# Kernel optimization log

Hardware: AMD Instinct MI355X
Metric: run time of the kernel (lower is better)

Reference implementation:

```python
import jax, jax.numpy as jnp
import numpy as np

B, N, F_IN, OUT_FEATS, NUM_CLS, NUM_INDS = 256, 200, 200, 256, 8, 512
PCT_EDGES = 20
K = int(PCT_EDGES / 100 * N * (N - 1) / 2)  # 3980 hard edges
TAU = 1.0


def setup_inputs() -> dict:
    key = jax.random.key(0)
    ks = jax.random.split(key, 6)
    x = jax.random.normal(ks[0], (B, N, F_IN), dtype=jnp.float32)
    gumbel_u = jax.random.uniform(ks[1], (B, N, N), dtype=jnp.float32)
    nets = jax.random.normal(ks[2], (NUM_INDS, N, N), dtype=jnp.float32)
    w_gnn = jax.random.normal(ks[3], (F_IN, OUT_FEATS), dtype=jnp.float32) / np.sqrt(F_IN).astype(np.float32)
    w_lin = jax.random.normal(ks[4], (OUT_FEATS, NUM_CLS), dtype=jnp.float32) / np.sqrt(OUT_FEATS).astype(np.float32)
    b_lin = jnp.zeros((NUM_CLS,), dtype=jnp.float32)
    net_index = jax.random.randint(ks[5], (B,), 0, NUM_INDS)
    return {"x": x, "gumbel_u": gumbel_u, "nets": nets, "w_gnn": w_gnn,
            "w_lin": w_lin, "b_lin": b_lin, "net_index": net_index}


def _gumbel_softkmax(logits, u, k, tau):
    # logits: [B, N, N]; u: uniform(0,1) noise -> Gumbel(0,1) via -log(-log(u))
    b, n, _ = logits.shape
    g = -jnp.log(-jnp.log(jnp.clip(u, 1e-10, 1.0 - 1e-10)))
    g = (logits + g) / tau
    sym = (g + jnp.swapaxes(g, 1, 2)) * 0.5                      # symmetrize
    y_soft = jax.nn.softmax(sym.reshape(b, -1), axis=-1).reshape(b, n, n)
    upper_flat = jnp.triu(y_soft).reshape(b, -1)                 # upper tri incl. diag
    _, idx = jax.lax.top_k(upper_flat, k)                        # [B, k]
    y_hard = jnp.zeros_like(upper_flat).at[jnp.arange(b)[:, None], idx].set(1.0)
    y_hard = y_hard.reshape(b, n, n)
    diag = jnp.diagonal(y_hard, axis1=-2, axis2=-1)              # [B, N]
    eye = jnp.eye(n, dtype=y_hard.dtype)
    y_hard = y_hard + jnp.swapaxes(y_hard, 1, 2) - diag[:, :, None] * eye
    # straight-through estimator
    return y_hard - jax.lax.stop_gradient(y_soft) + y_soft


def reference(x, gumbel_u, nets, w_gnn, w_lin, b_lin, net_index):
    selected = nets[net_index]                                   # [B, N, N]
    adj = _gumbel_softkmax(selected, gumbel_u, K, TAU)
    # gnn: relu(adj @ x @ W_gnn)  -> embeddings [B, N, OUT_FEATS]
    emb = jax.nn.relu(jnp.einsum('bij,bjf,fo->bio', adj, x, w_gnn))
    out = emb @ w_lin + b_lin                                    # [B, N, NUM_CLS]
    return out, emb, adj
```

## Files before the change

kernel.cpp:

```cpp
#include <hip/hip_runtime.h>
#include <math.h>

#define B_SZ 256
#define N_SZ 200
#define NN (N_SZ * N_SZ)
#define FIN 200
#define OUT_F 256
#define NCLS 8
#define KSEL 3980
#define NUPPER 20100
#define KSTRIDE 20128
#define NT 7
#define NTILES 28
#define CAND_CAP 2048

#define ADJ_STRIDE 224
#define KGRP_PB 25
#define XWM_PB (KGRP_PB * 2048)

#define EMB_OFF (B_SZ * N_SZ * NCLS)
#define ADJ_OFF (EMB_OFF + B_SZ * N_SZ * OUT_F)

#define KEYS_OFF_B   0
#define SEL_OFF_B    21659648
#define CCNT_OFF_B   21661696
#define CAND_OFF_B   21662720
#define WKG_OFF_B    26214400
#define ADJB16_OFF_B 26329088

typedef unsigned short ushort_t;
typedef float f32x4 __attribute__((ext_vector_type(4)));
typedef short bf16x8 __attribute__((ext_vector_type(8)));
typedef ushort_t u16x4 __attribute__((ext_vector_type(4)));

__device__ __forceinline__ unsigned sortkey(float f) {
    unsigned u = __float_as_uint(f);
    return (u & 0x80000000u) ? ~u : (u | 0x80000000u);
}

__device__ __forceinline__ ushort_t f2b(float f) {
    unsigned u = __float_as_uint(f);
    return (ushort_t)((u + 0x7FFFu + ((u >> 16) & 1u)) >> 16);
}

__device__ __forceinline__ bf16x8 f2b8(float4 lo, float4 hi) {
    bf16x8 r;
    r[0] = (short)f2b(lo.x); r[1] = (short)f2b(lo.y);
    r[2] = (short)f2b(lo.z); r[3] = (short)f2b(lo.w);
    r[4] = (short)f2b(hi.x); r[5] = (short)f2b(hi.y);
    r[6] = (short)f2b(hi.z); r[7] = (short)f2b(hi.w);
    return r;
}

__device__ __forceinline__ void tile_decode(int t, int& ti, int& tj) {
    int a = 0, rem = t;
    while (rem >= NT - a) { rem -= NT - a; ++a; }
    ti = a; tj = a + rem;
}

__global__ __launch_bounds__(256) void kA(
    const float* __restrict__ gu, const float* __restrict__ nets,
    const int* __restrict__ net_index, unsigned* __restrict__ keys,
    const float* __restrict__ wg, ushort_t* __restrict__ wkg,
    unsigned* __restrict__ candCnt)
{
    const int blk = blockIdx.x;
    if (blk >= B_SZ * NTILES) {
        int pb = blk - B_SZ * NTILES;
        if (pb == 0) candCnt[threadIdx.x] = 0;
        int e = pb * 256 + threadIdx.x;
        int kg = e >> 11;
        int rem = e & 2047;
        int n = rem >> 3;
        int ki = rem & 7;
        int k = kg * 8 + ki;
        wkg[e] = (k < FIN) ? f2b(wg[k * OUT_F + n]) : (ushort_t)0;
        return;
    }
    const int b = blk / NTILES;
    int ti, tj; tile_decode(blk % NTILES, ti, tj);
    const int i0 = ti * 32, j0 = tj * 32;
    const float* ub = gu + (size_t)b * NN;
    const float* lb = nets + (size_t)net_index[b] * NN;

    __shared__ float Hij[32][33];
    __shared__ float Hji[32][33];

    const int r = threadIdx.x >> 5;
    const int c = threadIdx.x & 31;

    #pragma unroll
    for (int s = 0; s < 4; ++s) {
        int rr = r + 8 * s;
        int i = i0 + rr, j = j0 + c;
        if (i < N_SZ && j < N_SZ) {
            float u = ub[i * N_SZ + j];
            u = fminf(fmaxf(u, 1e-10f), 1.0f - 1e-10f);
            Hij[rr][c] = lb[i * N_SZ + j] - logf(-logf(u));
        }
        if (ti != tj) {
            int i2 = j0 + rr, j2 = i0 + c;
            if (i2 < N_SZ && j2 < N_SZ) {
                float u = ub[i2 * N_SZ + j2];
                u = fminf(fmaxf(u, 1e-10f), 1.0f - 1e-10f);
                Hji[rr][c] = lb[i2 * N_SZ + j2] - logf(-logf(u));
            }
        }
    }
    __syncthreads();

    unsigned* kb = keys + (size_t)b * KSTRIDE;
    #pragma unroll
    for (int s = 0; s < 4; ++s) {
        int rr = r + 8 * s;
        int i = i0 + rr, j = j0 + c;
        if (i < N_SZ && j < N_SZ && i <= j) {
            float hji = (ti == tj) ? Hij[c][rr] : Hji[c][rr];
            float sv = 0.5f * (Hij[rr][c] + hji);
            int base = i * N_SZ - (i * (i - 1)) / 2;
            kb[base + (j - i)] = sortkey(sv);
        }
    }
}

__global__ __launch_bounds__(256) void kFinal(
    const unsigned* __restrict__ keys, unsigned* __restrict__ sel)
{
    const int b = blockIdx.x;
    const int tid = threadIdx.x;
    __shared__ unsigned kl[NUPPER];
    __shared__ unsigned hist[256];
    __shared__ unsigned sfx[256];
    __shared__ unsigned sPrefix;
    __shared__ int sKK;

    const unsigned* kb = keys + (size_t)b * KSTRIDE;
    for (int idx = tid; idx < NUPPER; idx += 256) kl[idx] = kb[idx];

    unsigned prefix = 0;
    int kk = KSEL;
    for (int round = 0; round < 4; ++round) {
        const int shift = 24 - 8 * round;
        hist[tid] = 0;
        __syncthreads();
        for (int idx = tid; idx < NUPPER; idx += 256) {
            unsigned key = kl[idx];
            bool in = (round == 0) || ((key >> (shift + 8)) == prefix);
            if (in) atomicAdd(&hist[(key >> shift) & 255u], 1u);
        }
        __syncthreads();
        sfx[tid] = hist[tid];
        __syncthreads();
        #pragma unroll
        for (int off = 1; off < 256; off <<= 1) {
            unsigned add = (tid + off < 256) ? sfx[tid + off] : 0u;
            __syncthreads();
            sfx[tid] += add;
            __syncthreads();
        }
        unsigned above = (tid < 255) ? sfx[tid + 1] : 0u;
        if (sfx[tid] >= (unsigned)kk && above < (unsigned)kk) {
            sPrefix = (prefix << 8) | (unsigned)tid;
            sKK = kk - (int)above;
        }
        __syncthreads();
        prefix = sPrefix;
        kk = sKK;
        __syncthreads();
    }
    if (tid == 0) {
        sel[b * 2] = prefix;
        sel[b * 2 + 1] = (unsigned)kk;
    }
}

__global__ __launch_bounds__(256) void kW(
    const unsigned* __restrict__ keys, const unsigned* __restrict__ sel,
    unsigned* __restrict__ candCnt, unsigned* __restrict__ cand,
    float* __restrict__ out_base, ushort_t* __restrict__ adjb16)
{
    const int blk = blockIdx.x;
    const int b = blk / NTILES;
    int ti, tj; tile_decode(blk % NTILES, ti, tj);
    const int i0 = ti * 32, j0 = tj * 32;
    const unsigned kth = sel[b * 2];
    const unsigned* kb = keys + (size_t)b * KSTRIDE;
    float* adj = out_base + ADJ_OFF + (size_t)b * NN;
    ushort_t* ab = adjb16 + (size_t)b * (N_SZ * ADJ_STRIDE);

    __shared__ float V[32][33];
    const int r = threadIdx.x >> 5;
    const int c = threadIdx.x & 31;

    #pragma unroll
    for (int s = 0; s < 4; ++s) {
        int rr = r + 8 * s;
        int i = i0 + rr, j = j0 + c;
        if (i < N_SZ && j < N_SZ && i <= j) {
            int base = i * N_SZ - (i * (i - 1)) / 2;
            unsigned key = kb[base + (j - i)];
            float v = (key > kth) ? 1.0f : 0.0f;
            if (key == kth) {
                unsigned p = atomicAdd(&candCnt[b], 1u);
                if (p < CAND_CAP) cand[(size_t)b * CAND_CAP + p] = (unsigned)(i * N_SZ + j);
            }
            V[rr][c] = v;
            if (ti == tj) V[c][rr] = v;
        }
    }
    __syncthreads();

    const int tr = threadIdx.x >> 3;
    const int tc = threadIdx.x & 7;
    {
        int i = i0 + tr;
        if (i < N_SZ) {
            int jb = j0 + tc * 4;
            float v0 = (jb + 0 < N_SZ) ? V[tr][tc * 4 + 0] : 0.0f;
            float v1 = (jb + 1 < N_SZ) ? V[tr][tc * 4 + 1] : 0.0f;
            float v2 = (jb + 2 < N_SZ) ? V[tr][tc * 4 + 2] : 0.0f;
            float v3 = (jb + 3 < N_SZ) ? V[tr][tc * 4 + 3] : 0.0f;
            if (jb + 3 < N_SZ) {
                float4 v4 = {v0, v1, v2, v3};
                *(float4*)(adj + (size_t)i * N_SZ + jb) = v4;
            } else {
                if (jb + 0 < N_SZ) adj[(size_t)i * N_SZ + jb + 0] = v0;
                if (jb + 1 < N_SZ) adj[(size_t)i * N_SZ + jb + 1] = v1;
                if (jb + 2 < N_SZ) adj[(size_t)i * N_SZ + jb + 2] = v2;
            }
            u16x4 a4;
            a4[0] = (v0 != 0.0f) ? (ushort_t)0x3F80 : (ushort_t)0;
            a4[1] = (v1 != 0.0f) ? (ushort_t)0x3F80 : (ushort_t)0;
            a4[2] = (v2 != 0.0f) ? (ushort_t)0x3F80 : (ushort_t)0;
            a4[3] = (v3 != 0.0f) ? (ushort_t)0x3F80 : (ushort_t)0;
            *(u16x4*)(ab + (size_t)i * ADJ_STRIDE + jb) = a4;
        }
    }
    if (ti != tj) {
        int i2 = j0 + tr;
        if (i2 < N_SZ) {
            int jb = i0 + tc * 4;
            float v0 = V[tc * 4 + 0][tr];
            float v1 = V[tc * 4 + 1][tr];
            float v2 = V[tc * 4 + 2][tr];
            float v3 = V[tc * 4 + 3][tr];
            float4 v4 = {v0, v1, v2, v3};
            *(float4*)(adj + (size_t)i2 * N_SZ + jb) = v4;
            u16x4 a4;
            a4[0] = (v0 != 0.0f) ? (ushort_t)0x3F80 : (ushort_t)0;
            a4[1] = (v1 != 0.0f) ? (ushort_t)0x3F80 : (ushort_t)0;
            a4[2] = (v2 != 0.0f) ? (ushort_t)0x3F80 : (ushort_t)0;
            a4[3] = (v3 != 0.0f) ? (ushort_t)0x3F80 : (ushort_t)0;
            *(u16x4*)(ab + (size_t)i2 * ADJ_STRIDE + jb) = a4;
        }
    }
}

__global__ void kT(const unsigned* __restrict__ sel,
                   const unsigned* __restrict__ candCnt,
                   const unsigned* __restrict__ cand,
                   float* __restrict__ out_base, ushort_t* __restrict__ adjb16)
{
    const int b = blockIdx.x;
    if (threadIdx.x != 0) return;
    int kk = (int)sel[b * 2 + 1];
    int cnt = (int)candCnt[b];
    if (cnt > CAND_CAP) cnt = CAND_CAP;
    float* adj = out_base + ADJ_OFF + (size_t)b * NN;
    ushort_t* ab = adjb16 + (size_t)b * (N_SZ * ADJ_STRIDE);
    int take = kk < cnt ? kk : cnt;
    unsigned used[64];
    int nu = 0;
    for (int t = 0; t < take; ++t) {
        unsigned best = 0xFFFFFFFFu;
        for (int q = 0; q < cnt; ++q) {
            unsigned v = cand[(size_t)b * CAND_CAP + q];
            bool skip = false;
            for (int u = 0; u < nu; ++u) if (used[u] == v) { skip = true; break; }
            if (!skip && v < best) best = v;
        }
        if (best == 0xFFFFFFFFu) break;
        if (nu < 64) used[nu++] = best;
        int i = (int)(best / N_SZ), j = (int)(best % N_SZ);
        adj[i * N_SZ + j] = 1.0f;
        adj[j * N_SZ + i] = 1.0f;
        ab[i * ADJ_STRIDE + j] = (ushort_t)0x3F80;
        ab[j * ADJ_STRIDE + i] = (ushort_t)0x3F80;
    }
}

__global__ __launch_bounds__(256) void k2_mfma(
    const float* __restrict__ x, const ushort_t* __restrict__ wkg,
    ushort_t* __restrict__ xwm)
{
    const int r0 = blockIdx.x * 64;
    const int tid = threadIdx.x;
    const int w = tid >> 6;
    const int l = tid & 63;
    const int g = l >> 4;
    const int r = l & 15;

    __shared__ __align__(16) ushort_t Cs[64 * 256];

    f32x4 acc[4][4];
    #pragma unroll
    for (int mf = 0; mf < 4; ++mf)
        #pragma unroll
        for (int nf = 0; nf < 4; ++nf)
            acc[mf][nf] = (f32x4){0.f, 0.f, 0.f, 0.f};

    for (int c = 0; c < 7; ++c) {
        const int koff = (c * 32 + g * 8 < FIN) ? (c * 32 + g * 8) : 0;
        bf16x8 af[4], bf[4];
        #pragma unroll
        for (int mf = 0; mf < 4; ++mf) {
            const float* ap = x + (size_t)(r0 + mf * 16 + r) * FIN + koff;
            float4 lo = *(const float4*)ap;
            float4 hi = *(const float4*)(ap + 4);
            af[mf] = f2b8(lo, hi);
        }
        #pragma unroll
        for (int nf = 0; nf < 4; ++nf)
            bf[nf] = *(const bf16x8*)(wkg + c * 8192 + g * 2048 + (w * 64 + nf * 16 + r) * 8);
        #pragma unroll
        for (int mf = 0; mf < 4; ++mf)
            #pragma unroll
            for (int nf = 0; nf < 4; ++nf)
                acc[mf][nf] = __builtin_amdgcn_mfma_f32_16x16x32_bf16(
                    af[mf], bf[nf], acc[mf][nf], 0, 0, 0);
    }

    #pragma unroll
    for (int mf = 0; mf < 4; ++mf) {
        #pragma unroll
        for (int jj = 0; jj < 4; ++jj) {
            int row = mf * 16 + g * 4 + jj;
            #pragma unroll
            for (int nf = 0; nf < 4; ++nf) {
                int col = w * 64 + nf * 16 + r;
                Cs[((row >> 3) << 11) + col * 8 + (row & 7)] = f2b(acc[mf][nf][jj]);
            }
        }
    }
    __syncthreads();
    #pragma unroll
    for (int kg = 0; kg < 8; ++kg) {
        int grow0 = r0 + kg * 8;
        int bb = grow0 / N_SZ;
        int jb = grow0 % N_SZ;
        ushort_t* dst = xwm + (size_t)bb * XWM_PB + ((jb >> 3) << 11);
        *(int4*)(dst + tid * 8) = *(const int4*)(Cs + (kg << 11) + tid * 8);
    }
}

__global__ __launch_bounds__(256) void k3_fused(
    const ushort_t* __restrict__ adjb16, const ushort_t* __restrict__ xwm,
    const float* __restrict__ wl, const float* __restrict__ bl,
    float* __restrict__ out_base)
{
    const int blk = blockIdx.x;
    const int xcd = blk & 7;
    const int idx = blk >> 3;
    const int b = xcd + 8 * (idx / 7);
    const int mt = idx % 7;
    const int tid = threadIdx.x;
    const int w = tid >> 6;
    const int l = tid & 63;
    const int g = l >> 4;
    const int r = l & 15;

    const ushort_t* adjb = adjb16 + (size_t)b * (N_SZ * ADJ_STRIDE);
    const ushort_t* xwb = xwm + (size_t)b * XWM_PB;

    __shared__ __align__(16) float Es[32 * 256];
    float (*red)[4][8][8] = (float(*)[4][8][8])Es;

    int arow0 = mt * 32 + r;       if (arow0 > N_SZ - 1) arow0 = N_SZ - 1;
    int arow1 = mt * 32 + 16 + r;  if (arow1 > N_SZ - 1) arow1 = N_SZ - 1;
    bf16x8 aa[2][7];
    #pragma unroll
    for (int c = 0; c < 7; ++c) {
        aa[0][c] = *(const bf16x8*)(adjb + arow0 * ADJ_STRIDE + c * 32 + g * 8);
        aa[1][c] = *(const bf16x8*)(adjb + arow1 * ADJ_STRIDE + c * 32 + g * 8);
    }

    f32x4 acc[2][4];
    #pragma unroll
    for (int mf = 0; mf < 2; ++mf)
        #pragma unroll
        for (int nf = 0; nf < 4; ++nf)
            acc[mf][nf] = (f32x4){0.f, 0.f, 0.f, 0.f};

    #pragma unroll
    for (int c = 0; c < 7; ++c) {
        bf16x8 bf[4];
        #pragma unroll
        for (int nf = 0; nf < 4; ++nf)
            bf[nf] = *(const bf16x8*)(xwb + c * 8192 + g * 2048 + (w * 64 + nf * 16 + r) * 8);
        #pragma unroll
        for (int mf = 0; mf < 2; ++mf)
            #pragma unroll
            for (int nf = 0; nf < 4; ++nf)
                acc[mf][nf] = __builtin_amdgcn_mfma_f32_16x16x32_bf16(
                    aa[mf][c], bf[nf], acc[mf][nf], 0, 0, 0);
    }

    #pragma unroll
    for (int mf = 0; mf < 2; ++mf) {
        #pragma unroll
        for (int j = 0; j < 4; ++j) {
            int rowl = mf * 16 + g * 4 + j;
            #pragma unroll
            for (int nf = 0; nf < 4; ++nf)
                Es[rowl * 256 + w * 64 + nf * 16 + r] = fmaxf(acc[mf][nf][j], 0.0f);
        }
    }
    __syncthreads();
    #pragma unroll
    for (int q = 0; q < 8; ++q) {
        int e = q * 256 + tid;
        int rowl = e >> 6;
        int c4 = e & 63;
        int grow = mt * 32 + rowl;
        if (grow < N_SZ) {
            float4 v = *(const float4*)(Es + rowl * 256 + c4 * 4);
            *(float4*)(out_base + EMB_OFF + ((size_t)b * N_SZ + grow) * OUT_F + c4 * 4) = v;
        }
    }
    __syncthreads();

    float wlv[4][NCLS];
    #pragma unroll
    for (int nf = 0; nf < 4; ++nf) {
        int col = w * 64 + nf * 16 + r;
        #pragma unroll
        for (int cls = 0; cls < NCLS; ++cls) wlv[nf][cls] = wl[col * NCLS + cls];
    }
    #pragma unroll
    for (int mf = 0; mf < 2; ++mf) {
        #pragma unroll
        for (int j = 0; j < 4; ++j) {
            float e0 = fmaxf(acc[mf][0][j], 0.0f);
            float e1 = fmaxf(acc[mf][1][j], 0.0f);
            float e2 = fmaxf(acc[mf][2][j], 0.0f);
            float e3 = fmaxf(acc[mf][3][j], 0.0f);
            float pr[NCLS];
            #pragma unroll
            for (int cls = 0; cls < NCLS; ++cls)
                pr[cls] = e0 * wlv[0][cls] + e1 * wlv[1][cls]
                        + e2 * wlv[2][cls] + e3 * wlv[3][cls];
            #pragma unroll
            for (int off = 1; off <= 8; off <<= 1) {
                #pragma unroll
                for (int cls = 0; cls < NCLS; ++cls)
                    pr[cls] += __shfl_xor(pr[cls], off, 64);
            }
            if (r < NCLS) red[w][g][mf * 4 + j][r] = pr[r];
        }
    }
    __syncthreads();

    {
        int rowl = tid >> 3, cls = tid & 7;
        int mf = rowl >> 4, rem = rowl & 15, gg = rem >> 2, jj = rem & 3;
        int slot = mf * 4 + jj;
        int grow = mt * 32 + rowl;
        if (grow < N_SZ) {
            float s = red[0][gg][slot][cls] + red[1][gg][slot][cls]
                    + red[2][gg][slot][cls] + red[3][gg][slot][cls] + bl[cls];
            out_base[((size_t)b * N_SZ + grow) * NCLS + cls] = s;
        }
    }
}

extern "C" void kernel_launch(void* const* d_in, const int* in_sizes, int n_in,
                              void* d_out, int out_size, void* d_ws, size_t ws_size,
                              hipStream_t stream) {
    const float* x    = (const float*)d_in[0];
    const float* gu   = (const float*)d_in[1];
    const float* nets = (const float*)d_in[2];
    const float* wg   = (const float*)d_in[3];
    const float* wl   = (const float*)d_in[4];
    const float* bl   = (const float*)d_in[5];
    const int*   nidx = (const int*)d_in[6];
    float* out = (float*)d_out;

    char* ws = (char*)d_ws;
    unsigned* keys    = (unsigned*)(ws + KEYS_OFF_B);
    unsigned* sel     = (unsigned*)(ws + SEL_OFF_B);
    unsigned* candCnt = (unsigned*)(ws + CCNT_OFF_B);
    unsigned* cand    = (unsigned*)(ws + CAND_OFF_B);
    ushort_t* xwm     = (ushort_t*)(ws + KEYS_OFF_B);
    ushort_t* wkg     = (ushort_t*)(ws + WKG_OFF_B);
    ushort_t* adjb16  = (ushort_t*)(ws + ADJB16_OFF_B);

    kA<<<B_SZ * NTILES + 224, 256, 0, stream>>>(gu, nets, nidx, keys, wg, wkg, candCnt);
    kFinal<<<B_SZ, 256, 0, stream>>>(keys, sel);
    kW<<<B_SZ * NTILES, 256, 0, stream>>>(keys, sel, candCnt, cand, out, adjb16);
    kT<<<B_SZ, 64, 0, stream>>>(sel, candCnt, cand, out, adjb16);

    k2_mfma<<<(B_SZ * N_SZ) / 64, 256, 0, stream>>>(x, wkg, xwm);
    k3_fused<<<B_SZ * 7, 256, 0, stream>>>(adjb16, xwm, wl, bl, out);
}
```

Measured before the change: 148.4 us.

## Fuse x@W and adj@(xW) GEMMs into one per-batch kernel via LDS

Merges the two GEMM kernels into a single kernel with one block per batch. The block computes x@W_gnn for all 200 rows into registers, stages the bf16 result in swizzled shared memory, then multiplies by the adjacency and writes the embeddings and logits directly. This drops the global round trip of the intermediate xW and one launch. In exchange the grid shrinks to 256 large blocks with heavy register use (two 13x4 accumulator sets) and ~118KB of LDS, which limits occupancy and latency hiding. Embedding stores are now scalar and no longer staged through LDS.

Measured after the change: 224.1 us. +51.0%, slower.

```diff
diff --git a/kernel.cpp b/kernel.cpp
--- a/kernel.cpp
+++ b/kernel.cpp
@@ -15,8 +15,6 @@
 #define CAND_CAP 2048
 
 #define ADJ_STRIDE 224
-#define KGRP_PB 25
-#define XWM_PB (KGRP_PB * 2048)
 
 #define EMB_OFF (B_SZ * N_SZ * NCLS)
 #define ADJ_OFF (EMB_OFF + B_SZ * N_SZ * OUT_F)
@@ -41,15 +39,6 @@
 __device__ __forceinline__ ushort_t f2b(float f) {
     unsigned u = __float_as_uint(f);
     return (ushort_t)((u + 0x7FFFu + ((u >> 16) & 1u)) >> 16);
-}
-
-__device__ __forceinline__ bf16x8 f2b8(float4 lo, float4 hi) {
-    bf16x8 r;
-    r[0] = (short)f2b(lo.x); r[1] = (short)f2b(lo.y);
-    r[2] = (short)f2b(lo.z); r[3] = (short)f2b(lo.w);
-    r[4] = (short)f2b(hi.x); r[5] = (short)f2b(hi.y);
-    r[6] = (short)f2b(hi.z); r[7] = (short)f2b(hi.w);
-    return r;
 }
 
 __device__ __forceinline__ void tile_decode(int t, int& ti, int& tj) {
@@ -289,145 +278,145 @@
     }
 }
 
-__global__ __launch_bounds__(256) void k2_mfma(
+__global__ __launch_bounds__(256, 1) void k23(
     const float* __restrict__ x, const ushort_t* __restrict__ wkg,
-    ushort_t* __restrict__ xwm)
+    const ushort_t* __restrict__ adjb16, const float* __restrict__ wl,
+    const float* __restrict__ bl, float* __restrict__ out_base)
 {
-    const int r0 = blockIdx.x * 64;
+    const int b = blockIdx.x;
     const int tid = threadIdx.x;
     const int w = tid >> 6;
     const int l = tid & 63;
     const int g = l >> 4;
     const int r = l & 15;
 
-    __shared__ __align__(16) ushort_t Cs[64 * 256];
-
-    f32x4 acc[4][4];
-    #pragma unroll
-    for (int mf = 0; mf < 4; ++mf)
+    __shared__ __align__(16) char pool[118400];
+    ushort_t* Axs = (ushort_t*)(pool + 102400);
+
+    const float* xb = x + (size_t)b * (N_SZ * FIN);
+    const ushort_t* adjb = adjb16 + (size_t)b * (N_SZ * ADJ_STRIDE);
+
+    f32x4 acc1[13][4];
+    #pragma unroll
+    for (int mf = 0; mf < 13; ++mf)
         #pragma unroll
         for (int nf = 0; nf < 4; ++nf)
-            acc[mf][nf] = (f32x4){0.f, 0.f, 0.f, 0.f};
+            acc1[mf][nf] = (f32x4){0.f, 0.f, 0.f, 0.f};
+
+    float4 xr[7];
+    #pragma unroll
+    for (int i = 0; i < 7; ++i) {
+        int q = i * 256 + tid;
+        if (q < 1600)
+            xr[i] = *(const float4*)(xb + (size_t)(q >> 3) * FIN + (q & 7) * 4);
+    }
 
     for (int c = 0; c < 7; ++c) {
-        const int koff = (c * 32 + g * 8 < FIN) ? (c * 32 + g * 8) : 0;
-        bf16x8 af[4], bf[4];
-        #pragma unroll
-        for (int mf = 0; mf < 4; ++mf) {
-            const float* ap = x + (size_t)(r0 + mf * 16 + r) * FIN + koff;
-            float4 lo = *(const float4*)ap;
-            float4 hi = *(const float4*)(ap + 4);
-            af[mf] = f2b8(lo, hi);
-        }
+        __syncthreads();
+        #pragma unroll
+        for (int i = 0; i < 7; ++i) {
+            int q = i * 256 + tid;
+            if (q < 1600) {
+                int row = q >> 3, c4 = q & 7;
+                u16x4 v4;
+                v4[0] = f2b(xr[i].x); v4[1] = f2b(xr[i].y);
+                v4[2] = f2b(xr[i].z); v4[3] = f2b(xr[i].w);
+                *(u16x4*)(Axs + row * 40 + c4 * 4) = v4;
+            }
+        }
+        __syncthreads();
+        if (c < 6) {
+            int cn = c + 1;
+            #pragma unroll
+            for (int i = 0; i < 7; ++i) {
+                int q = i * 256 + tid;
+                if (q < 1600) {
+                    int col = cn * 32 + (q & 7) * 4;
+                    if (col < FIN)
+                        xr[i] = *(const float4*)(xb + (size_t)(q >> 3) * FIN + col);
+                    else
+                        xr[i] = (float4){0.f, 0.f, 0.f, 0.f};
+                }
+            }
+        }
+        bf16x8 bf[4];
         #pragma unroll
         for (int nf = 0; nf < 4; ++nf)
             bf[nf] = *(const bf16x8*)(wkg + c * 8192 + g * 2048 + (w * 64 + nf * 16 + r) * 8);
         #pragma unroll
-        for (int mf = 0; mf < 4; ++mf)
+        for (int mf = 0; mf < 13; ++mf) {
+            int row = mf * 16 + r; if (row > N_SZ - 1) row = N_SZ - 1;
+            bf16x8 af = *(const bf16x8*)(Axs + row * 40 + g * 8);
             #pragma unroll
             for (int nf = 0; nf < 4; ++nf)
-                acc[mf][nf] = __builtin_amdgcn_mfma_f32_16x16x32_bf16(
-                    af[mf], bf[nf], acc[mf][nf], 0, 0, 0);
-    }
-
-    #pragma unroll
-    for (int mf = 0; mf < 4; ++mf) {
-        #pragma unroll
-        for (int jj = 0; jj < 4; ++jj) {
-            int row = mf * 16 + g * 4 + jj;
-            #pragma unroll
-            for (int nf = 0; nf < 4; ++nf) {
-                int col = w * 64 + nf * 16 + r;
-                Cs[((row >> 3) << 11) + col * 8 + (row & 7)] = f2b(acc[mf][nf][jj]);
-            }
-        }
-    }
-    __syncthreads();
-    #pragma unroll
-    for (int kg = 0; kg < 8; ++kg) {
-        int grow0 = r0 + kg * 8;
-        int bb = grow0 / N_SZ;
-        int jb = grow0 % N_SZ;
-        ushort_t* dst = xwm + (size_t)bb * XWM_PB + ((jb >> 3) << 11);
-        *(int4*)(dst + tid * 8) = *(const int4*)(Cs + (kg << 11) + tid * 8);
-    }
-}
-
-__global__ __launch_bounds__(256) void k3_fused(
-    const ushort_t* __restrict__ adjb16, const ushort_t* __restrict__ xwm,
-    const float* __restrict__ wl, const float* __restrict__ bl,
-    float* __restrict__ out_base)
-{
-    const int blk = blockIdx.x;
-    const int xcd = blk & 7;
-    const int idx = blk >> 3;
-    const int b = xcd + 8 * (idx / 7);
-    const int mt = idx % 7;
-    const int tid = threadIdx.x;
-    const int w = tid >> 6;
-    const int l = tid & 63;
-    const int g = l >> 4;
-    const int r = l & 15;
-
-    const ushort_t* adjb = adjb16 + (size_t)b * (N_SZ * ADJ_STRIDE);
-    const ushort_t* xwb = xwm + (size_t)b * XWM_PB;
-
-    __shared__ __align__(16) float Es[32 * 256];
-    float (*red)[4][8][8] = (float(*)[4][8][8])Es;
-
-    int arow0 = mt * 32 + r;       if (arow0 > N_SZ - 1) arow0 = N_SZ - 1;
-    int arow1 = mt * 32 + 16 + r;  if (arow1 > N_SZ - 1) arow1 = N_SZ - 1;
-    bf16x8 aa[2][7];
+                acc1[mf][nf] = __builtin_amdgcn_mfma_f32_16x16x32_bf16(
+                    af, bf[nf], acc1[mf][nf], 0, 0, 0);
+        }
+    }
+
+    __syncthreads();
+    #pragma unroll
+    for (int mf = 0; mf < 13; ++mf) {
+        #pragma unroll
+        for (int j = 0; j < 4; ++j) {
+            int row = mf * 16 + g * 4 + j;
+            if (row < N_SZ) {
+                int kg = row >> 3;
+                int ki = row & 7;
+                #pragma unroll
+                for (int nf = 0; nf < 4; ++nf) {
+                    int col = w * 64 + nf * 16 + r;
+                    int byte = kg * 4096 + ((col ^ (kg & 7)) << 4) + ki * 2;
+                    *(ushort_t*)(pool + byte) = f2b(acc1[mf][nf][j]);
+                }
+            }
+        }
+    }
+    __syncthreads();
+
+    f32x4 acc2[13][4];
+    #pragma unroll
+    for (int mf = 0; mf < 13; ++mf)
+        #pragma unroll
+        for (int nf = 0; nf < 4; ++nf)
+            acc2[mf][nf] = (f32x4){0.f, 0.f, 0.f, 0.f};
+
+    bf16x8 ar[2][13];
+    #pragma unroll
+    for (int mf = 0; mf < 13; ++mf) {
+        int row = mf * 16 + r; if (row > N_SZ - 1) row = N_SZ - 1;
+        ar[0][mf] = *(const bf16x8*)(adjb + row * ADJ_STRIDE + g * 8);
+    }
     #pragma unroll
     for (int c = 0; c < 7; ++c) {
-        aa[0][c] = *(const bf16x8*)(adjb + arow0 * ADJ_STRIDE + c * 32 + g * 8);
-        aa[1][c] = *(const bf16x8*)(adjb + arow1 * ADJ_STRIDE + c * 32 + g * 8);
-    }
-
-    f32x4 acc[2][4];
-    #pragma unroll
-    for (int mf = 0; mf < 2; ++mf)
-        #pragma unroll
-        for (int nf = 0; nf < 4; ++nf)
-            acc[mf][nf] = (f32x4){0.f, 0.f, 0.f, 0.f};
-
-    #pragma unroll
-    for (int c = 0; c < 7; ++c) {
+        if (c < 6) {
+            #pragma unroll
+            for (int mf = 0; mf < 13; ++mf) {
+                int row = mf * 16 + r; if (row > N_SZ - 1) row = N_SZ - 1;
+                ar[(c + 1) & 1][mf] =
+                    *(const bf16x8*)(adjb + row * ADJ_STRIDE + (c + 1) * 32 + g * 8);
+            }
+        }
+        int kgrp = c * 4 + g;
         bf16x8 bf[4];
         #pragma unroll
-        for (int nf = 0; nf < 4; ++nf)
-            bf[nf] = *(const bf16x8*)(xwb + c * 8192 + g * 2048 + (w * 64 + nf * 16 + r) * 8);
-        #pragma unroll
-        for (int mf = 0; mf < 2; ++mf)
+        for (int nf = 0; nf < 4; ++nf) {
+            int n = w * 64 + nf * 16 + r;
+            bf16x8 bv = (bf16x8){0, 0, 0, 0, 0, 0, 0, 0};
+            if (kgrp < 25)
+                bv = *(const bf16x8*)(pool + kgrp * 4096 + ((n ^ (kgrp & 7)) << 4));
+            bf[nf] = bv;
+        }
+        #pragma unroll
+        for (int mf = 0; mf < 13; ++mf)
             #pragma unroll
             for (int nf = 0; nf < 4; ++nf)
-                acc[mf][nf] = __builtin_amdgcn_mfma_f32_16x16x32_bf16(
-                    aa[mf][c], bf[nf], acc[mf][nf], 0, 0, 0);
-    }
-
-    #pragma unroll
-    for (int mf = 0; mf < 2; ++mf) {
-        #pragma unroll
-        for (int j = 0; j < 4; ++j) {
-            int rowl = mf * 16 + g * 4 + j;
-            #pragma unroll
-            for (int nf = 0; nf < 4; ++nf)
-                Es[rowl * 256 + w * 64 + nf * 16 + r] = fmaxf(acc[mf][nf][j], 0.0f);
-        }
-    }
-    __syncthreads();
-    #pragma unroll
-    for (int q = 0; q < 8; ++q) {
-        int e = q * 256 + tid;
-        int rowl = e >> 6;
-        int c4 = e & 63;
-        int grow = mt * 32 + rowl;
-        if (grow < N_SZ) {
-            float4 v = *(const float4*)(Es + rowl * 256 + c4 * 4);
-            *(float4*)(out_base + EMB_OFF + ((size_t)b * N_SZ + grow) * OUT_F + c4 * 4) = v;
-        }
-    }
-    __syncthreads();
+                acc2[mf][nf] = __builtin_amdgcn_mfma_f32_16x16x32_bf16(
+                    ar[c & 1][mf], bf[nf], acc2[mf][nf], 0, 0, 0);
+    }
+    __syncthreads();
+
+    float (*red)[4][52][8] = (float(*)[4][52][8])pool;
 
     float wlv[4][NCLS];
     #pragma unroll
@@ -436,14 +425,23 @@
         #pragma unroll
         for (int cls = 0; cls < NCLS; ++cls) wlv[nf][cls] = wl[col * NCLS + cls];
     }
-    #pragma unroll
-    for (int mf = 0; mf < 2; ++mf) {
+
+    #pragma unroll
+    for (int mf = 0; mf < 13; ++mf) {
         #pragma unroll
         for (int j = 0; j < 4; ++j) {
-            float e0 = fmaxf(acc[mf][0][j], 0.0f);
-            float e1 = fmaxf(acc[mf][1][j], 0.0f);
-            float e2 = fmaxf(acc[mf][2][j], 0.0f);
-            float e3 = fmaxf(acc[mf][3][j], 0.0f);
+            int row = mf * 16 + g * 4 + j;
+            float e0 = fmaxf(acc2[mf][0][j], 0.0f);
+            float e1 = fmaxf(acc2[mf][1][j], 0.0f);
+            float e2 = fmaxf(acc2[mf][2][j], 0.0f);
+            float e3 = fmaxf(acc2[mf][3][j], 0.0f);
+            if (row < N_SZ) {
+                size_t rbase = EMB_OFF + ((size_t)b * N_SZ + row) * OUT_F;
+                out_base[rbase + w * 64 + r]      = e0;
+                out_base[rbase + w * 64 + 16 + r] = e1;
+                out_base[rbase + w * 64 + 32 + r] = e2;
+                out_base[rbase + w * 64 + 48 + r] = e3;
+            }
             float pr[NCLS];
             #pragma unroll
             for (int cls = 0; cls < NCLS; ++cls)
@@ -460,16 +458,13 @@
     }
     __syncthreads();
 
-    {
-        int rowl = tid >> 3, cls = tid & 7;
-        int mf = rowl >> 4, rem = rowl & 15, gg = rem >> 2, jj = rem & 3;
+    for (int e = tid; e < N_SZ * NCLS; e += 256) {
+        int row = e >> 3, cls = e & 7;
+        int mf = row >> 4, rr = row & 15, gg = rr >> 2, jj = rr & 3;
         int slot = mf * 4 + jj;
-        int grow = mt * 32 + rowl;
-        if (grow < N_SZ) {
-            float s = red[0][gg][slot][cls] + red[1][gg][slot][cls]
-                    + red[2][gg][slot][cls] + red[3][gg][slot][cls] + bl[cls];
-            out_base[((size_t)b * N_SZ + grow) * NCLS + cls] = s;
-        }
+        float s = red[0][gg][slot][cls] + red[1][gg][slot][cls]
+                + red[2][gg][slot][cls] + red[3][gg][slot][cls] + bl[cls];
+        out_base[((size_t)b * N_SZ + row) * NCLS + cls] = s;
     }
 }
 
@@ -490,7 +485,6 @@
     unsigned* sel     = (unsigned*)(ws + SEL_OFF_B);
     unsigned* candCnt = (unsigned*)(ws + CCNT_OFF_B);
     unsigned* cand    = (unsigned*)(ws + CAND_OFF_B);
-    ushort_t* xwm     = (ushort_t*)(ws + KEYS_OFF_B);
     ushort_t* wkg     = (ushort_t*)(ws + WKG_OFF_B);
     ushort_t* adjb16  = (ushort_t*)(ws + ADJB16_OFF_B);
 
@@ -498,7 +492,5 @@
     kFinal<<<B_SZ, 256, 0, stream>>>(keys, sel);
     kW<<<B_SZ * NTILES, 256, 0, stream>>>(keys, sel, candCnt, cand, out, adjb16);
     kT<<<B_SZ, 64, 0, stream>>>(sel, candCnt, cand, out, adjb16);
-
-    k2_mfma<<<(B_SZ * N_SZ) / 64, 256, 0, stream>>>(x, wkg, xwm);
-    k3_fused<<<B_SZ * 7, 256, 0, stream>>>(adjb16, xwm, wl, bl, out);
-}
+    k23<<<B_SZ, 256, 0, stream>>>(x, wkg, adjb16, wl, bl, out);
+}
```
